# Kernel optimization log

Measured on AMD Instinct MI355X. Metric: run time of the kernel, lower is better.

Reference implementation:

```python
import jax, jax.numpy as jnp
import numpy as np

EMBED, HEAD, CTX = 1024, 64, 2048

def setup_inputs() -> dict:
    key = jax.random.key(0)
    k1, k2, k3, k4 = jax.random.split(key, 4)
    x = jax.random.normal(k1, (16, 2048, EMBED), dtype=jnp.float32)
    s = EMBED ** -0.5  # torch Linear default init scale-ish
    Wq = jax.random.normal(k2, (EMBED, HEAD), dtype=jnp.float32) * s
    Wk = jax.random.normal(k3, (EMBED, HEAD), dtype=jnp.float32) * s
    Wv = jax.random.normal(k4, (EMBED, HEAD), dtype=jnp.float32) * s
    return {"x": x, "Wq": Wq, "Wk": Wk, "Wv": Wv}

def reference(x, Wq, Wk, Wv):
    # x: [B, S, E] -> q,k,v: [B, S, H]
    q = jnp.einsum('bse,eh->bsh', x, Wq)
    k = jnp.einsum('bse,eh->bsh', x, Wk)
    v = jnp.einsum('bse,eh->bsh', x, Wv)
    scale = k.shape[-1] ** -0.5
    scores = jnp.einsum('bqh,bkh->bqk', q, k) * scale  # [B, S, S]
    S = x.shape[1]
    causal = jnp.tril(jnp.ones((S, S), dtype=bool))
    scores = jnp.where(causal, scores, -jnp.inf)
    attn = jax.nn.softmax(scores, axis=-1)
    return jnp.einsum('bqk,bkh->bqh', attn, v)  # [B, S, H]
```

## Files before the change

### kernel.cpp

```cpp
#include <hip/hip_runtime.h>
#include <hip/hip_bf16.h>
#include <math.h>

#define BATCH 16
#define SEQ   2048
#define EMB   1024
#define HD    64
#define NROWS (BATCH*SEQ)

typedef __attribute__((ext_vector_type(8))) short short8;
typedef __attribute__((ext_vector_type(4))) float f32x4;

#define SWZ(byte, row)   ((byte) ^ (((row) & 7) << 4))
#define SWZ16(byte, row) ((byte) ^ (((row) & 15) << 4))

__device__ __forceinline__ ushort f2bf(float f) {
    union { float f; unsigned u; } c; c.f = f;
    return (ushort)((c.u + 0x7FFF + ((c.u >> 16) & 1)) >> 16);
}

__device__ __forceinline__ unsigned pk2bf(float a, float b) {
    union { __hip_bfloat162 h; unsigned u; } c;
    c.h = __float22bfloat162_rn(make_float2(a, b));
    return c.u;
}

__device__ __forceinline__ void gload_lds16(const void* g, void* l) {
    __builtin_amdgcn_global_load_lds(
        (const __attribute__((address_space(1))) void*)g,
        (__attribute__((address_space(3))) void*)l, 16, 0, 0);
}

__global__ void k_transpose_w(const float* __restrict__ Wq,
                              const float* __restrict__ Wk,
                              const float* __restrict__ Wv,
                              ushort* __restrict__ wt) {
    int idx  = blockIdx.x * 256 + threadIdx.x;
    int c192 = idx >> 10;
    int e    = idx & 1023;
    const float* W = (c192 < 64) ? Wq : (c192 < 128 ? Wk : Wv);
    wt[idx] = f2bf(W[e * HD + (c192 & 63)]);
}

__global__ __launch_bounds__(256)
void k_qkv_proj(const float* __restrict__ x, const ushort* __restrict__ wt,
                ushort* __restrict__ qkv, ushort* __restrict__ vt) {
    __shared__ short8 smem[49152 / 16];
    char* base = (char*)smem;
    const int t = threadIdx.x, lane = t & 63, w = t >> 6;
    const int l15 = lane & 15, lg = lane >> 4;
    const int row0 = blockIdx.x * 64;
    const float* xrowp = x + (size_t)(row0 + w * 16 + l15) * EMB;

    f32x4 acc[12];
    #pragma unroll
    for (int mi = 0; mi < 12; ++mi) acc[mi] = (f32x4){0.f, 0.f, 0.f, 0.f};

    float4 xc[4], xn[4];

    auto stage_w = [&](int ch, int buf) {
        char* wb = base + buf * 24576;
        #pragma unroll
        for (int i = 0; i < 6; ++i) {
            int r = (w * 6 + i) * 8 + (lane >> 3);
            int j = (lane & 7) ^ (r & 7);
            gload_lds16(&wt[(size_t)r * EMB + ch * 64 + j * 8],
                        wb + (w * 6 + i) * 1024);
        }
    };
    auto load_x = [&](int ch, float4* xr) {
        #pragma unroll
        for (int s = 0; s < 2; ++s) {
            const float* p = xrowp + ch * 64 + s * 32 + lg * 8;
            xr[s * 2 + 0] = *(const float4*)(p);
            xr[s * 2 + 1] = *(const float4*)(p + 4);
        }
    };

    stage_w(0, 0); load_x(0, xc);
    #pragma unroll 2
    for (int ch = 0; ch < 16; ++ch) {
        int cur = ch & 1;
        if (ch < 15) {
            stage_w(ch + 1, cur ^ 1); load_x(ch + 1, xn);
            asm volatile("s_waitcnt vmcnt(10)" ::: "memory");
        } else {
            asm volatile("s_waitcnt vmcnt(0)" ::: "memory");
        }
        __builtin_amdgcn_sched_barrier(0);
        __builtin_amdgcn_s_barrier();
        char* wb = base + cur * 24576;
        #pragma unroll
        for (int s = 0; s < 2; ++s) {
            const float* xp = (const float*)&xc[s * 2];
            short8 xf;
            #pragma unroll
            for (int e = 0; e < 8; ++e) xf[e] = (short)f2bf(xp[e]);
            __builtin_amdgcn_s_setprio(1);
            #pragma unroll
            for (int mi = 0; mi < 12; ++mi) {
                int cr = mi * 16 + l15;
                short8 wf = *(short8*)(wb + SWZ(cr * 128 + s * 64 + lg * 16, cr));
                acc[mi] = (mi < 8)
                    ? __builtin_amdgcn_mfma_f32_16x16x32_bf16(wf, xf, acc[mi], 0, 0, 0)
                    : __builtin_amdgcn_mfma_f32_16x16x32_bf16(xf, wf, acc[mi], 0, 0, 0);
            }
            __builtin_amdgcn_s_setprio(0);
        }
        if (ch < 15) {
            #pragma unroll
            for (int i = 0; i < 4; ++i) xc[i] = xn[i];
        }
        __builtin_amdgcn_sched_barrier(0);
        __builtin_amdgcn_s_barrier();
    }

    char* qkb = base;
    char* vtb = base + 16384;
    const float qscale = 0.125f * 1.44269504f;
    #pragma unroll
    for (int mi = 0; mi < 12; ++mi) {
        ushort4 o;
        if (mi < 8) {
            float sc = (mi < 4) ? qscale : 1.0f;
            o.x = f2bf(acc[mi][0] * sc); o.y = f2bf(acc[mi][1] * sc);
            o.z = f2bf(acc[mi][2] * sc); o.w = f2bf(acc[mi][3] * sc);
            int xrow = w * 16 + l15, c = mi * 16 + lg * 4;
            *(ushort4*)(qkb + SWZ16(xrow * 256 + c * 2, xrow)) = o;
        } else {
            o.x = f2bf(acc[mi][0]); o.y = f2bf(acc[mi][1]);
            o.z = f2bf(acc[mi][2]); o.w = f2bf(acc[mi][3]);
            int hd = (mi - 8) * 16 + l15, key = w * 16 + lg * 4;
            *(ushort4*)(vtb + SWZ(hd * 128 + key * 2, hd)) = o;
        }
    }
    __syncthreads();
    const int b = row0 >> 11, r0b = row0 & 2047;
    #pragma unroll
    for (int i = 0; i < 4; ++i) {
        int idx = t + i * 256;
        int r = idx >> 4, g = idx & 15;
        short8 v = *(short8*)(qkb + SWZ16(r * 256 + g * 16, r));
        int c0 = g * 8, m = c0 >> 6, c = c0 & 63;
        *(short8*)&qkv[((size_t)m * NROWS + row0 + r) * HD + c] = v;
    }
    #pragma unroll
    for (int i = 0; i < 2; ++i) {
        int idx = t + i * 256;
        int hd = idx >> 3, g = idx & 7;
        short8 v = *(short8*)(vtb + SWZ(hd * 128 + g * 16, hd));
        *(short8*)&vt[((size_t)b * HD + hd) * SEQ + r0b + g * 8] = v;
    }
}

__global__ __launch_bounds__(256)
void k_attn(const ushort* __restrict__ q, const ushort* __restrict__ k,
            const ushort* __restrict__ vt, float* __restrict__ out) {
    __shared__ short8 smem[40960 / 16];
    char* base = (char*)smem;
    char* pls  = base + 32768;
    const int t = threadIdx.x, lane = t & 63, w = t >> 6;
    const int l15 = lane & 15, lg = lane >> 4;
    const int b = blockIdx.x & 15;
    const int j = blockIdx.x >> 4;
    const int qt = (j < 16) ? (31 - j) : (j - 16);
    const int row0 = qt * 64, r0w = row0 + w * 16;
    const ushort* qb = q  + (size_t)b * SEQ * HD;
    const ushort* kb = k  + (size_t)b * SEQ * HD;
    const ushort* vb = vt + (size_t)b * HD * SEQ;
    char* pw = pls + w * 2048;

    short8 qf[2];
    #pragma unroll
    for (int s = 0; s < 2; ++s)
        qf[s] = *(const short8*)&qb[(size_t)(r0w + l15) * HD + s * 32 + lg * 8];

    f32x4 oacc[4];
    #pragma unroll
    for (int h = 0; h < 4; ++h) oacc[h] = (f32x4){0.f, 0.f, 0.f, 0.f};
    float m_ = -INFINITY, l_ = 0.f;

    auto stage = [&](int kt, int buf) {
        char* kbuf = base + buf * 16384;
        char* vbuf = kbuf + 8192;
        int k0 = kt * 64;
        #pragma unroll
        for (int g = 0; g < 2; ++g) {
            int rk = w * 16 + g * 8 + (lane >> 3);
            int jk = (lane & 7) ^ (rk & 7);
            gload_lds16(&kb[(size_t)(k0 + rk) * HD + jk * 8],
                        kbuf + (w * 2 + g) * 1024);
            int rv = w * 16 + g * 8 + (lane >> 3);
            int jv = (lane & 7) ^ (rv & 7);
            gload_lds16(&vb[(size_t)rv * SEQ + k0 + jv * 8],
                        vbuf + (w * 2 + g) * 1024);
        }
    };

    const int nkt = qt + 1;
    stage(0, 0);
    for (int kt = 0; kt < nkt; ++kt) {
        int cur = kt & 1;
        if (kt + 1 < nkt) {
            stage(kt + 1, cur ^ 1);
            asm volatile("s_waitcnt vmcnt(4)" ::: "memory");
        } else {
            asm volatile("s_waitcnt vmcnt(0)" ::: "memory");
        }
        __builtin_amdgcn_sched_barrier(0);
        __builtin_amdgcn_s_barrier();
        char* kls = base + cur * 16384;
        char* vls = kls + 8192;
        int k0 = kt * 64;

        f32x4 sa[4];
        #pragma unroll
        for (int a = 0; a < 4; ++a) sa[a] = (f32x4){0.f, 0.f, 0.f, 0.f};
        __builtin_amdgcn_s_setprio(1);
        #pragma unroll
        for (int s = 0; s < 2; ++s)
            #pragma unroll
            for (int a = 0; a < 4; ++a) {
                int r = a * 16 + l15;
                short8 kf = *(short8*)(kls + SWZ(r * 128 + s * 64 + lg * 16, r));
                sa[a] = __builtin_amdgcn_mfma_f32_16x16x32_bf16(kf, qf[s], sa[a], 0, 0, 0);
            }
        __builtin_amdgcn_s_setprio(0);

        if (kt == nkt - 1) {
            int qrow = r0w + l15;
            #pragma unroll
            for (int a = 0; a < 4; ++a)
                #pragma unroll
                for (int r = 0; r < 4; ++r)
                    if (k0 + a * 16 + lg * 4 + r > qrow) sa[a][r] = -INFINITY;
        }

        float ma[4];
        #pragma unroll
        for (int a = 0; a < 4; ++a)
            ma[a] = fmaxf(fmaxf(sa[a][0], sa[a][1]), fmaxf(sa[a][2], sa[a][3]));
        float mx = fmaxf(fmaxf(ma[0], ma[1]), fmaxf(ma[2], ma[3]));
        mx = fmaxf(mx, __shfl_xor(mx, 16));
        mx = fmaxf(mx, __shfl_xor(mx, 32));
        if (!__all(mx - m_ <= 8.0f)) {
            float mn   = fmaxf(m_, mx);
            float corr = __builtin_amdgcn_exp2f(m_ - mn);
            l_ *= corr;
            #pragma unroll
            for (int h = 0; h < 4; ++h) oacc[h] *= corr;
            m_ = mn;
        }
        float p[16];
        #pragma unroll
        for (int a = 0; a < 4; ++a)
            #pragma unroll
            for (int r = 0; r < 4; ++r)
                p[a * 4 + r] = __builtin_amdgcn_exp2f(sa[a][r] - m_);
        float ps = 0.f;
        #pragma unroll
        for (int a = 0; a < 4; ++a)
            ps += (p[a * 4 + 0] + p[a * 4 + 1]) + (p[a * 4 + 2] + p[a * 4 + 3]);
        l_ += ps;

        #pragma unroll
        for (int a = 0; a < 4; ++a) {
            uint2 pb;
            pb.x = pk2bf(p[a * 4 + 0], p[a * 4 + 1]);
            pb.y = pk2bf(p[a * 4 + 2], p[a * 4 + 3]);
            *(uint2*)(pw + SWZ(l15 * 128 + a * 32 + lg * 8, l15)) = pb;
        }

        __builtin_amdgcn_s_setprio(1);
        #pragma unroll
        for (int ki = 0; ki < 2; ++ki) {
            short8 pf = *(short8*)(pw + SWZ(l15 * 128 + ki * 64 + lg * 16, l15));
            #pragma unroll
            for (int h = 0; h < 4; ++h) {
                int rr = h * 16 + l15;
                short8 vf = *(short8*)(vls + SWZ(rr * 128 + ki * 64 + lg * 16, rr));
                oacc[h] = __builtin_amdgcn_mfma_f32_16x16x32_bf16(vf, pf, oacc[h], 0, 0, 0);
            }
        }
        __builtin_amdgcn_s_setprio(0);
        __builtin_amdgcn_sched_barrier(0);
        __builtin_amdgcn_s_barrier();
    }

    l_ += __shfl_xor(l_, 16);
    l_ += __shfl_xor(l_, 32);
    float inv = 1.0f / l_;
    #pragma unroll
    for (int h = 0; h < 4; ++h) {
        f32x4 v = oacc[h] * inv;
        int qr = w * 16 + l15;
        *(f32x4*)(base + SWZ16(qr * 256 + h * 64 + lg * 16, qr)) = v;
    }
    __syncthreads();
    #pragma unroll
    for (int i = 0; i < 4; ++i) {
        int idx = t + i * 256;
        int r = idx >> 4, g = idx & 15;
        f32x4 v = *(f32x4*)(base + SWZ16(r * 256 + g * 16, r));
        *(f32x4*)&out[((size_t)b * SEQ + row0 + r) * HD + g * 4] = v;
    }
}

extern "C" void kernel_launch(void* const* d_in, const int* in_sizes, int n_in,
                              void* d_out, int out_size, void* d_ws, size_t ws_size,
                              hipStream_t stream) {
    const float* x  = (const float*)d_in[0];
    const float* Wq = (const float*)d_in[1];
    const float* Wk = (const float*)d_in[2];
    const float* Wv = (const float*)d_in[3];
    float* out = (float*)d_out;
    ushort* ws = (ushort*)d_ws;
    ushort* wt16 = ws;
    ushort* qk16 = ws + 192 * 1024;
    ushort* vt16 = qk16 + (size_t)2 * NROWS * HD;

    k_transpose_w<<<768, 256, 0, stream>>>(Wq, Wk, Wv, wt16);
    k_qkv_proj  <<<NROWS / 64, 256, 0, stream>>>(x, wt16, qk16, vt16);
    k_attn      <<<BATCH * (SEQ / 64), 256, 0, stream>>>(
                    qk16, qk16 + (size_t)NROWS * HD, vt16, out);
}
```

Measured before the change: 70.90 us.

## Split each causal query tile's KV range across two blocks with atomic merge

Each query tile's key range is split into two halves processed by separate blocks, doubling the attention grid. Each block writes its unnormalized partial output and its running max and sum to workspace. An atomic counter lets the second finisher combine both partials with log-sum-exp rescaling and write the final output. This targets load imbalance and low occupancy from the causal triangle, in exchange for extra global traffic, fences and a counter reset in the transpose kernel.

```diff
diff --git a/kernel.cpp b/kernel.cpp
--- a/kernel.cpp
+++ b/kernel.cpp
@@ -7,6 +7,7 @@
 #define EMB   1024
 #define HD    64
 #define NROWS (BATCH*SEQ)
+#define MINF  (-1e30f)
 
 typedef __attribute__((ext_vector_type(8))) short short8;
 typedef __attribute__((ext_vector_type(4))) float f32x4;
@@ -34,7 +35,9 @@
 __global__ void k_transpose_w(const float* __restrict__ Wq,
                               const float* __restrict__ Wk,
                               const float* __restrict__ Wv,
-                              ushort* __restrict__ wt) {
+                              ushort* __restrict__ wt,
+                              unsigned* __restrict__ cnt) {
+    if (blockIdx.x < 2) cnt[blockIdx.x * 256 + threadIdx.x] = 0;
     int idx  = blockIdx.x * 256 + threadIdx.x;
     int c192 = idx >> 10;
     int e    = idx & 1023;
@@ -155,15 +158,19 @@
 
 __global__ __launch_bounds__(256)
 void k_attn(const ushort* __restrict__ q, const ushort* __restrict__ k,
-            const ushort* __restrict__ vt, float* __restrict__ out) {
+            const ushort* __restrict__ vt, float* __restrict__ out,
+            float* __restrict__ po, float* __restrict__ pml,
+            unsigned* __restrict__ cnt) {
     __shared__ short8 smem[40960 / 16];
+    __shared__ unsigned sflag;
     char* base = (char*)smem;
     char* pls  = base + 32768;
     const int t = threadIdx.x, lane = t & 63, w = t >> 6;
     const int l15 = lane & 15, lg = lane >> 4;
     const int b = blockIdx.x & 15;
-    const int j = blockIdx.x >> 4;
-    const int qt = (j < 16) ? (31 - j) : (j - 16);
+    const int u = blockIdx.x >> 4;
+    const int qt = 31 - (u >> 1);
+    const int s  = u & 1;
     const int row0 = qt * 64, r0w = row0 + w * 16;
     const ushort* qb = q  + (size_t)b * SEQ * HD;
     const ushort* kb = k  + (size_t)b * SEQ * HD;
@@ -172,13 +179,13 @@
 
     short8 qf[2];
     #pragma unroll
-    for (int s = 0; s < 2; ++s)
-        qf[s] = *(const short8*)&qb[(size_t)(r0w + l15) * HD + s * 32 + lg * 8];
+    for (int sx = 0; sx < 2; ++sx)
+        qf[sx] = *(const short8*)&qb[(size_t)(r0w + l15) * HD + sx * 32 + lg * 8];
 
     f32x4 oacc[4];
     #pragma unroll
     for (int h = 0; h < 4; ++h) oacc[h] = (f32x4){0.f, 0.f, 0.f, 0.f};
-    float m_ = -INFINITY, l_ = 0.f;
+    float m_ = MINF, l_ = 0.f;
 
     auto stage = [&](int kt, int buf) {
         char* kbuf = base + buf * 16384;
@@ -197,11 +204,15 @@
         }
     };
 
-    const int nkt = qt + 1;
-    stage(0, 0);
-    for (int kt = 0; kt < nkt; ++kt) {
-        int cur = kt & 1;
-        if (kt + 1 < nkt) {
+    const int nkt  = qt + 1;
+    const int half = (nkt + 1) >> 1;
+    const int k_lo = s ? half : 0;
+    const int k_hi = s ? nkt  : half;
+
+    if (k_lo < k_hi) stage(k_lo, 0);
+    for (int kt = k_lo; kt < k_hi; ++kt) {
+        int cur = (kt - k_lo) & 1;
+        if (kt + 1 < k_hi) {
             stage(kt + 1, cur ^ 1);
             asm volatile("s_waitcnt vmcnt(4)" ::: "memory");
         } else {
@@ -218,12 +229,12 @@
         for (int a = 0; a < 4; ++a) sa[a] = (f32x4){0.f, 0.f, 0.f, 0.f};
         __builtin_amdgcn_s_setprio(1);
         #pragma unroll
-        for (int s = 0; s < 2; ++s)
+        for (int sx = 0; sx < 2; ++sx)
             #pragma unroll
             for (int a = 0; a < 4; ++a) {
                 int r = a * 16 + l15;
-                short8 kf = *(short8*)(kls + SWZ(r * 128 + s * 64 + lg * 16, r));
-                sa[a] = __builtin_amdgcn_mfma_f32_16x16x32_bf16(kf, qf[s], sa[a], 0, 0, 0);
+                short8 kf = *(short8*)(kls + SWZ(r * 128 + sx * 64 + lg * 16, r));
+                sa[a] = __builtin_amdgcn_mfma_f32_16x16x32_bf16(kf, qf[sx], sa[a], 0, 0, 0);
             }
         __builtin_amdgcn_s_setprio(0);
 
@@ -289,20 +300,34 @@
 
     l_ += __shfl_xor(l_, 16);
     l_ += __shfl_xor(l_, 32);
-    float inv = 1.0f / l_;
+
+    const int  slot  = ((b * 32 + qt) << 1) | s;
+    const int  pslot = slot ^ 1;
+    float* po_s = po + (size_t)slot * 4096;
+    #pragma unroll
+    for (int h = 0; h < 4; ++h)
+        *(f32x4*)&po_s[(w * 16 + l15) * 64 + h * 16 + lg * 4] = oacc[h];
+    if (lg == 0)
+        *(float2*)&pml[(size_t)slot * 128 + (w * 16 + l15) * 2] = make_float2(m_, l_);
+    __threadfence();
+    __syncthreads();
+    if (t == 0) sflag = atomicAdd(&cnt[b * 32 + qt], 1u);
+    __syncthreads();
+    if (sflag == 0) return;
+    __threadfence();
+
+    const float* po_p = po + (size_t)pslot * 4096;
+    float2 mlp = *(const float2*)&pml[(size_t)pslot * 128 + (w * 16 + l15) * 2];
+    float M   = fmaxf(m_, mlp.x);
+    float ss_ = __builtin_amdgcn_exp2f(m_ - M);
+    float sp_ = __builtin_amdgcn_exp2f(mlp.x - M);
+    float inv = 1.0f / (l_ * ss_ + mlp.y * sp_);
+    int qrow = r0w + l15;
     #pragma unroll
     for (int h = 0; h < 4; ++h) {
-        f32x4 v = oacc[h] * inv;
-        int qr = w * 16 + l15;
-        *(f32x4*)(base + SWZ16(qr * 256 + h * 64 + lg * 16, qr)) = v;
-    }
-    __syncthreads();
-    #pragma unroll
-    for (int i = 0; i < 4; ++i) {
-        int idx = t + i * 256;
-        int r = idx >> 4, g = idx & 15;
-        f32x4 v = *(f32x4*)(base + SWZ16(r * 256 + g * 16, r));
-        *(f32x4*)&out[((size_t)b * SEQ + row0 + r) * HD + g * 4] = v;
+        f32x4 opp = *(const f32x4*)&po_p[(w * 16 + l15) * 64 + h * 16 + lg * 4];
+        f32x4 o = (oacc[h] * ss_ + opp * sp_) * inv;
+        *(f32x4*)&out[((size_t)b * SEQ + qrow) * HD + h * 16 + lg * 4] = o;
     }
 }
 
@@ -318,9 +343,13 @@
     ushort* wt16 = ws;
     ushort* qk16 = ws + 192 * 1024;
     ushort* vt16 = qk16 + (size_t)2 * NROWS * HD;
-
-    k_transpose_w<<<768, 256, 0, stream>>>(Wq, Wk, Wv, wt16);
+    char* wsb = (char*)d_ws;
+    float*    po  = (float*)(wsb + 16u * 1024 * 1024);
+    float*    pml = (float*)(wsb + 33u * 1024 * 1024);
+    unsigned* cnt = (unsigned*)(wsb + 34u * 1024 * 1024);
+
+    k_transpose_w<<<768, 256, 0, stream>>>(Wq, Wk, Wv, wt16, cnt);
     k_qkv_proj  <<<NROWS / 64, 256, 0, stream>>>(x, wt16, qk16, vt16);
-    k_attn      <<<BATCH * (SEQ / 64), 256, 0, stream>>>(
-                    qk16, qk16 + (size_t)NROWS * HD, vt16, out);
-}
+    k_attn      <<<BATCH * 64, 256, 0, stream>>>(
+                    qk16, qk16 + (size_t)NROWS * HD, vt16, out, po, pml, cnt);
+}
```

After: 242.0 us. 3.41x slower.
